# Kernel optimization log

Hardware: AMD Instinct MI355X
Metric: run time of the kernel (lower is better)

Reference implementation:

```python
import jax, jax.numpy as jnp
import numpy as np

S = 2        # downscale
REDUCE = 32  # QK channel dim


def _to_grid(x):
    # [B,C,H,W] -> [B,C,H/S,W/S,S*S], matching ConverToGrid (reshape+permute+reshape)
    B, C, H, W = x.shape
    h, w = H // S, W // S
    x = x.reshape(B, C, h, S, w, S)
    x = x.transpose(0, 1, 2, 4, 3, 5)
    return x.reshape(B, C, h, w, S * S)


def setup_inputs() -> dict:
    key = jax.random.key(0)
    k1, k2, k3 = jax.random.split(key, 3)
    fm = jax.random.normal(k1, (8, 128, 256, 256), dtype=jnp.float32)
    Wq = jax.random.normal(k2, (REDUCE, 128), dtype=jnp.float32) * 0.05
    Wk = jax.random.normal(k3, (REDUCE, 128), dtype=jnp.float32) * 0.05
    return {"fm": fm, "Wq": Wq, "Wk": Wk}


def reference(fm, Wq, Wk):
    B, C, H, W = fm.shape
    h, w = H // S, W // S
    # Q branch: AvgPool2d(S,S) -> 1x1 conv -> scale by 1/sqrt(reduce)
    pooled = fm.reshape(B, C, h, S, w, S).mean(axis=(3, 5))          # [B,C,h,w]
    Q = jnp.einsum('rc,bchw->brhw', Wq, pooled) / jnp.sqrt(
        jnp.asarray(REDUCE, fm.dtype))                               # [B,r,h,w]
    # K branch: 1x1 conv -> grid
    K = _to_grid(jnp.einsum('rc,bchw->brhw', Wk, fm))                # [B,r,h,w,S*S]
    # V branch: grid of raw features
    V = _to_grid(fm)                                                 # [B,C,h,w,S*S]
    # sum over channel dim of Q*K, softmax over window dim (dropout p=0 => identity)
    logits = jnp.einsum('brhw,brhws->bhws', Q, K)                    # [B,h,w,S*S]
    attn = jax.nn.softmax(logits, axis=-1)
    # weighted sum over window positions
    out = jnp.einsum('bchws,bhws->bchw', V, attn)                    # [B,C,h,w]
    return out
```

## Files before the change

kernel.cpp:

```cpp
#include <hip/hip_runtime.h>
#include <hip/hip_bf16.h>
#include <math.h>


typedef unsigned int uint32;

__device__ __forceinline__ uint32 pack2(float x, float y) {
  union { __hip_bfloat162 h; uint32 u; } cvt;
  cvt.h = __float22bfloat162_rn(make_float2(x, y));
  return cvt.u;
}
__device__ __forceinline__ float2 unpack2(uint32 u) {
  float2 r;
  r.x = __uint_as_float(u << 16);
  r.y = __uint_as_float(u & 0xffff0000u);
  return r;
}

__global__ __launch_bounds__(256) void wt_kernel(const float* __restrict__ Wq,
                                                 const float* __restrict__ Wk,
                                                 float* __restrict__ ws) {
  int t = blockIdx.x * 256 + threadIdx.x;
  if (t < 4096) {
    int c = t >> 5, r = t & 31;
    ws[c * 32 + r]        = Wq[r * 128 + c] * (0.25f / sqrtf(32.0f));
    ws[4096 + c * 32 + r] = Wk[r * 128 + c];
  }
}

__global__ __launch_bounds__(512)
void attn_main(const float* __restrict__ fm,
               const float* __restrict__ ws,
               float* __restrict__ out) {
  __shared__ float Qpart[4 * 32 * 64];
  __shared__ float lbuf[8 * 64 * 4];
  __shared__ float abuf[64 * 4];

  const int tid = threadIdx.x;
  const int p   = tid & 63;
  const int g   = __builtin_amdgcn_readfirstlane(tid >> 6);

  const int blk = blockIdx.x;
  const int w0  = (blk & 1) * 64;
  const int h   = (blk >> 1) & 127;
  const int b   = blk >> 8;
  const int cb  = g * 16;

  const float* gbase = fm + ((size_t)(b * 128 + cb) * 65536) +
                       (size_t)(2 * h) * 256 + 2 * (w0 + p);
  const float* wq = ws + cb * 32;
  const float* wk = ws + 4096 + cb * 32;

  uint32 pka[16], pkb[16];
  {
    const float* gp = gbase;
#pragma unroll
    for (int i = 0; i < 16; ++i) {
      const float2 va = *(const float2*)(gp);
      const float2 vb = *(const float2*)(gp + 256);
      pka[i] = pack2(va.x, va.y);
      pkb[i] = pack2(vb.x, vb.y);
      gp += 65536;
    }
  }

  float qa[32];
#pragma unroll
  for (int r = 0; r < 32; ++r) qa[r] = 0.f;
#pragma unroll
  for (int i = 0; i < 16; ++i) {
    const float2 va = unpack2(pka[i]);
    const float2 vb = unpack2(pkb[i]);
    const float u = (va.x + va.y) + (vb.x + vb.y);
#pragma unroll
    for (int r = 0; r < 32; ++r)
      qa[r] = fmaf(wq[i * 32 + r], u, qa[r]);
  }

  if (g >= 4) {
#pragma unroll
    for (int r = 0; r < 32; ++r) Qpart[(g - 4) * 2048 + r * 64 + p] = qa[r];
  }
  __syncthreads();
  if (g < 4) {
#pragma unroll
    for (int r = 0; r < 32; ++r) Qpart[g * 2048 + r * 64 + p] += qa[r];
  }
  __syncthreads();
  if (g < 2) {
#pragma unroll
    for (int r = 0; r < 32; ++r)
      Qpart[g * 2048 + r * 64 + p] += Qpart[(g + 2) * 2048 + r * 64 + p];
  }
  __syncthreads();
#pragma unroll
  for (int r = 0; r < 32; ++r)
    qa[r] = Qpart[r * 64 + p] + Qpart[2048 + r * 64 + p];

  float l0 = 0.f, l1 = 0.f, l2 = 0.f, l3 = 0.f;
#pragma unroll
  for (int i = 0; i < 16; ++i) {
    const float2 va = unpack2(pka[i]);
    const float2 vb = unpack2(pkb[i]);
    float t0 = 0.f, t1 = 0.f;
#pragma unroll
    for (int r = 0; r < 32; r += 2) {
      t0 = fmaf(qa[r + 0], wk[i * 32 + r + 0], t0);
      t1 = fmaf(qa[r + 1], wk[i * 32 + r + 1], t1);
    }
    const float tv = t0 + t1;
    l0 = fmaf(tv, va.x, l0);
    l1 = fmaf(tv, va.y, l1);
    l2 = fmaf(tv, vb.x, l2);
    l3 = fmaf(tv, vb.y, l3);
  }
  *(float4*)(lbuf + (g * 64 + p) * 4) = make_float4(l0, l1, l2, l3);
  __syncthreads();

  if (tid < 64) {
    float L0 = 0.f, L1 = 0.f, L2 = 0.f, L3 = 0.f;
#pragma unroll
    for (int k = 0; k < 8; ++k) {
      const float4 s = *(const float4*)(lbuf + (k * 64 + tid) * 4);
      L0 += s.x; L1 += s.y; L2 += s.z; L3 += s.w;
    }
    const float mx = fmaxf(fmaxf(L0, L1), fmaxf(L2, L3));
    const float e0 = __expf(L0 - mx), e1 = __expf(L1 - mx);
    const float e2 = __expf(L2 - mx), e3 = __expf(L3 - mx);
    const float inv = 1.0f / ((e0 + e1) + (e2 + e3));
    *(float4*)(abuf + tid * 4) =
        make_float4(e0 * inv, e1 * inv, e2 * inv, e3 * inv);
  }
  __syncthreads();
  const float4 at = *(const float4*)(abuf + p * 4);

  {
    float* op = out + ((size_t)(b * 128 + cb) * 16384) + h * 128 + w0 + p;
#pragma unroll
    for (int i = 0; i < 16; ++i) {
      const float2 va = unpack2(pka[i]);
      const float2 vb = unpack2(pkb[i]);
      op[(size_t)i * 16384] =
          fmaf(at.x, va.x, fmaf(at.y, va.y, fmaf(at.z, vb.x, at.w * vb.y)));
    }
  }
}

extern "C" void kernel_launch(void* const* d_in, const int* in_sizes, int n_in,
                              void* d_out, int out_size, void* d_ws, size_t ws_size,
                              hipStream_t stream) {
  const float* fm = (const float*)d_in[0];
  const float* Wq = (const float*)d_in[1];
  const float* Wk = (const float*)d_in[2];
  float* outp = (float*)d_out;
  float* ws = (float*)d_ws;

  wt_kernel<<<16, 256, 0, stream>>>(Wq, Wk, ws);
  attn_main<<<2048, 512, 0, stream>>>(fm, ws, outp);
}
```

Baseline: 138.3 us.

## Split Q reduction into two 16-channel halves and shrink blocks to 32 pixels

Blocks now cover 32 output pixels with 256 threads (8 channel groups of 32 lanes) instead of 64 pixels with 512 threads, and launch bounds ask for 8 blocks per CU. The 32-channel Q accumulation is split into two 16-channel passes with separate shared reductions, which halves the live Q registers to raise occupancy. Weight reads are vectorized as float4. The cost is more barriers and a recomputed pooled sum per pass, and each wave now issues 32-lane memory accesses, so half of every 64-wide wavefront sits idle.

```diff
diff --git a/kernel.cpp b/kernel.cpp
--- a/kernel.cpp
+++ b/kernel.cpp
@@ -28,100 +28,199 @@
   }
 }
 
-__global__ __launch_bounds__(512)
+__global__ __launch_bounds__(256, 8)
 void attn_main(const float* __restrict__ fm,
                const float* __restrict__ ws,
                float* __restrict__ out) {
-  __shared__ float Qpart[4 * 32 * 64];
-  __shared__ float lbuf[8 * 64 * 4];
-  __shared__ float abuf[64 * 4];
+  __shared__ float QsA[4 * 16 * 32];
+  __shared__ float QsB[4 * 16 * 32];
 
   const int tid = threadIdx.x;
-  const int p   = tid & 63;
-  const int g   = __builtin_amdgcn_readfirstlane(tid >> 6);
+  const int p   = tid & 31;
+  const int cq  = tid >> 5;
 
   const int blk = blockIdx.x;
-  const int w0  = (blk & 1) * 64;
-  const int h   = (blk >> 1) & 127;
-  const int b   = blk >> 8;
-  const int cb  = g * 16;
-
-  const float* gbase = fm + ((size_t)(b * 128 + cb) * 65536) +
+  const int w0  = (blk & 3) * 32;
+  const int h   = (blk >> 2) & 127;
+  const int b   = blk >> 9;
+  const int cb  = cq * 16;
+
+  const float* gbase = fm + ((size_t)(b * 128 + cb)) * 65536 +
                        (size_t)(2 * h) * 256 + 2 * (w0 + p);
-  const float* wq = ws + cb * 32;
-  const float* wk = ws + 4096 + cb * 32;
+  const float* wqp = ws + cb * 32;
+  const float* wkp = ws + 4096 + cb * 32;
 
   uint32 pka[16], pkb[16];
-  {
-    const float* gp = gbase;
-#pragma unroll
-    for (int i = 0; i < 16; ++i) {
-      const float2 va = *(const float2*)(gp);
-      const float2 vb = *(const float2*)(gp + 256);
-      pka[i] = pack2(va.x, va.y);
-      pkb[i] = pack2(vb.x, vb.y);
-      gp += 65536;
-    }
-  }
-
-  float qa[32];
-#pragma unroll
-  for (int r = 0; r < 32; ++r) qa[r] = 0.f;
+#pragma unroll
+  for (int i = 0; i < 16; ++i) {
+    const float2 va = *(const float2*)(gbase + (size_t)i * 65536);
+    const float2 vb = *(const float2*)(gbase + (size_t)i * 65536 + 256);
+    pka[i] = pack2(va.x, va.y);
+    pkb[i] = pack2(vb.x, vb.y);
+  }
+
+  float qa[16];
+
+#pragma unroll
+  for (int r = 0; r < 16; ++r) qa[r] = 0.f;
 #pragma unroll
   for (int i = 0; i < 16; ++i) {
     const float2 va = unpack2(pka[i]);
     const float2 vb = unpack2(pkb[i]);
     const float u = (va.x + va.y) + (vb.x + vb.y);
-#pragma unroll
-    for (int r = 0; r < 32; ++r)
-      qa[r] = fmaf(wq[i * 32 + r], u, qa[r]);
-  }
-
-  if (g >= 4) {
-#pragma unroll
-    for (int r = 0; r < 32; ++r) Qpart[(g - 4) * 2048 + r * 64 + p] = qa[r];
-  }
-  __syncthreads();
-  if (g < 4) {
-#pragma unroll
-    for (int r = 0; r < 32; ++r) Qpart[g * 2048 + r * 64 + p] += qa[r];
-  }
-  __syncthreads();
-  if (g < 2) {
-#pragma unroll
-    for (int r = 0; r < 32; ++r)
-      Qpart[g * 2048 + r * 64 + p] += Qpart[(g + 2) * 2048 + r * 64 + p];
-  }
-  __syncthreads();
-#pragma unroll
-  for (int r = 0; r < 32; ++r)
-    qa[r] = Qpart[r * 64 + p] + Qpart[2048 + r * 64 + p];
-
-  float l0 = 0.f, l1 = 0.f, l2 = 0.f, l3 = 0.f;
+    const float4 w0_ = *(const float4*)(wqp + i * 32 + 0);
+    const float4 w1_ = *(const float4*)(wqp + i * 32 + 4);
+    const float4 w2_ = *(const float4*)(wqp + i * 32 + 8);
+    const float4 w3_ = *(const float4*)(wqp + i * 32 + 12);
+    qa[0]  = fmaf(w0_.x, u, qa[0]);
+    qa[1]  = fmaf(w0_.y, u, qa[1]);
+    qa[2]  = fmaf(w0_.z, u, qa[2]);
+    qa[3]  = fmaf(w0_.w, u, qa[3]);
+    qa[4]  = fmaf(w1_.x, u, qa[4]);
+    qa[5]  = fmaf(w1_.y, u, qa[5]);
+    qa[6]  = fmaf(w1_.z, u, qa[6]);
+    qa[7]  = fmaf(w1_.w, u, qa[7]);
+    qa[8]  = fmaf(w2_.x, u, qa[8]);
+    qa[9]  = fmaf(w2_.y, u, qa[9]);
+    qa[10] = fmaf(w2_.z, u, qa[10]);
+    qa[11] = fmaf(w2_.w, u, qa[11]);
+    qa[12] = fmaf(w3_.x, u, qa[12]);
+    qa[13] = fmaf(w3_.y, u, qa[13]);
+    qa[14] = fmaf(w3_.z, u, qa[14]);
+    qa[15] = fmaf(w3_.w, u, qa[15]);
+  }
+  if (cq >= 4) {
+#pragma unroll
+    for (int r = 0; r < 16; ++r) QsA[(cq - 4) * 512 + r * 32 + p] = qa[r];
+  }
+  __syncthreads();
+  if (cq < 4) {
+#pragma unroll
+    for (int r = 0; r < 16; ++r) QsA[cq * 512 + r * 32 + p] += qa[r];
+  }
+  __syncthreads();
+  if (cq < 2) {
+#pragma unroll
+    for (int r = 0; r < 16; ++r)
+      QsA[cq * 512 + r * 32 + p] += QsA[(cq + 2) * 512 + r * 32 + p];
+  }
+  __syncthreads();
+
+#pragma unroll
+  for (int r = 0; r < 16; ++r) qa[r] = 0.f;
 #pragma unroll
   for (int i = 0; i < 16; ++i) {
     const float2 va = unpack2(pka[i]);
     const float2 vb = unpack2(pkb[i]);
-    float t0 = 0.f, t1 = 0.f;
-#pragma unroll
-    for (int r = 0; r < 32; r += 2) {
-      t0 = fmaf(qa[r + 0], wk[i * 32 + r + 0], t0);
-      t1 = fmaf(qa[r + 1], wk[i * 32 + r + 1], t1);
-    }
-    const float tv = t0 + t1;
-    l0 = fmaf(tv, va.x, l0);
-    l1 = fmaf(tv, va.y, l1);
-    l2 = fmaf(tv, vb.x, l2);
-    l3 = fmaf(tv, vb.y, l3);
-  }
-  *(float4*)(lbuf + (g * 64 + p) * 4) = make_float4(l0, l1, l2, l3);
-  __syncthreads();
-
-  if (tid < 64) {
+    const float u = (va.x + va.y) + (vb.x + vb.y);
+    const float4 w0_ = *(const float4*)(wqp + i * 32 + 16);
+    const float4 w1_ = *(const float4*)(wqp + i * 32 + 20);
+    const float4 w2_ = *(const float4*)(wqp + i * 32 + 24);
+    const float4 w3_ = *(const float4*)(wqp + i * 32 + 28);
+    qa[0]  = fmaf(w0_.x, u, qa[0]);
+    qa[1]  = fmaf(w0_.y, u, qa[1]);
+    qa[2]  = fmaf(w0_.z, u, qa[2]);
+    qa[3]  = fmaf(w0_.w, u, qa[3]);
+    qa[4]  = fmaf(w1_.x, u, qa[4]);
+    qa[5]  = fmaf(w1_.y, u, qa[5]);
+    qa[6]  = fmaf(w1_.z, u, qa[6]);
+    qa[7]  = fmaf(w1_.w, u, qa[7]);
+    qa[8]  = fmaf(w2_.x, u, qa[8]);
+    qa[9]  = fmaf(w2_.y, u, qa[9]);
+    qa[10] = fmaf(w2_.z, u, qa[10]);
+    qa[11] = fmaf(w2_.w, u, qa[11]);
+    qa[12] = fmaf(w3_.x, u, qa[12]);
+    qa[13] = fmaf(w3_.y, u, qa[13]);
+    qa[14] = fmaf(w3_.z, u, qa[14]);
+    qa[15] = fmaf(w3_.w, u, qa[15]);
+  }
+  if (cq >= 4) {
+#pragma unroll
+    for (int r = 0; r < 16; ++r) QsB[(cq - 4) * 512 + r * 32 + p] = qa[r];
+  }
+  __syncthreads();
+  if (cq < 4) {
+#pragma unroll
+    for (int r = 0; r < 16; ++r) QsB[cq * 512 + r * 32 + p] += qa[r];
+  }
+  __syncthreads();
+  if (cq < 2) {
+#pragma unroll
+    for (int r = 0; r < 16; ++r)
+      QsB[cq * 512 + r * 32 + p] += QsB[(cq + 2) * 512 + r * 32 + p];
+  }
+  __syncthreads();
+
+  float l0 = 0.f, l1 = 0.f, l2 = 0.f, l3 = 0.f;
+  {
+    float qh[16];
+#pragma unroll
+    for (int r = 0; r < 16; ++r)
+      qh[r] = QsA[r * 32 + p] + QsA[512 + r * 32 + p];
+#pragma unroll
+    for (int i = 0; i < 16; ++i) {
+      const float4 k0 = *(const float4*)(wkp + i * 32 + 0);
+      const float4 k1 = *(const float4*)(wkp + i * 32 + 4);
+      const float4 k2 = *(const float4*)(wkp + i * 32 + 8);
+      const float4 k3 = *(const float4*)(wkp + i * 32 + 12);
+      float t0 = 0.f, t1 = 0.f;
+      t0 = fmaf(qh[0],  k0.x, t0); t1 = fmaf(qh[1],  k0.y, t1);
+      t0 = fmaf(qh[2],  k0.z, t0); t1 = fmaf(qh[3],  k0.w, t1);
+      t0 = fmaf(qh[4],  k1.x, t0); t1 = fmaf(qh[5],  k1.y, t1);
+      t0 = fmaf(qh[6],  k1.z, t0); t1 = fmaf(qh[7],  k1.w, t1);
+      t0 = fmaf(qh[8],  k2.x, t0); t1 = fmaf(qh[9],  k2.y, t1);
+      t0 = fmaf(qh[10], k2.z, t0); t1 = fmaf(qh[11], k2.w, t1);
+      t0 = fmaf(qh[12], k3.x, t0); t1 = fmaf(qh[13], k3.y, t1);
+      t0 = fmaf(qh[14], k3.z, t0); t1 = fmaf(qh[15], k3.w, t1);
+      const float tv = t0 + t1;
+      const float2 va = unpack2(pka[i]);
+      const float2 vb = unpack2(pkb[i]);
+      l0 = fmaf(tv, va.x, l0);
+      l1 = fmaf(tv, va.y, l1);
+      l2 = fmaf(tv, vb.x, l2);
+      l3 = fmaf(tv, vb.y, l3);
+    }
+  }
+  {
+    float qh[16];
+#pragma unroll
+    for (int r = 0; r < 16; ++r)
+      qh[r] = QsB[r * 32 + p] + QsB[512 + r * 32 + p];
+#pragma unroll
+    for (int i = 0; i < 16; ++i) {
+      const float4 k0 = *(const float4*)(wkp + i * 32 + 16);
+      const float4 k1 = *(const float4*)(wkp + i * 32 + 20);
+      const float4 k2 = *(const float4*)(wkp + i * 32 + 24);
+      const float4 k3 = *(const float4*)(wkp + i * 32 + 28);
+      float t0 = 0.f, t1 = 0.f;
+      t0 = fmaf(qh[0],  k0.x, t0); t1 = fmaf(qh[1],  k0.y, t1);
+      t0 = fmaf(qh[2],  k0.z, t0); t1 = fmaf(qh[3],  k0.w, t1);
+      t0 = fmaf(qh[4],  k1.x, t0); t1 = fmaf(qh[5],  k1.y, t1);
+      t0 = fmaf(qh[6],  k1.z, t0); t1 = fmaf(qh[7],  k1.w, t1);
+      t0 = fmaf(qh[8],  k2.x, t0); t1 = fmaf(qh[9],  k2.y, t1);
+      t0 = fmaf(qh[10], k2.z, t0); t1 = fmaf(qh[11], k2.w, t1);
+      t0 = fmaf(qh[12], k3.x, t0); t1 = fmaf(qh[13], k3.y, t1);
+      t0 = fmaf(qh[14], k3.z, t0); t1 = fmaf(qh[15], k3.w, t1);
+      const float tv = t0 + t1;
+      const float2 va = unpack2(pka[i]);
+      const float2 vb = unpack2(pkb[i]);
+      l0 = fmaf(tv, va.x, l0);
+      l1 = fmaf(tv, va.y, l1);
+      l2 = fmaf(tv, vb.x, l2);
+      l3 = fmaf(tv, vb.y, l3);
+    }
+  }
+  __syncthreads();
+
+  float* lbuf = QsA;
+  *(float4*)(lbuf + (cq * 32 + p) * 4) = make_float4(l0, l1, l2, l3);
+  __syncthreads();
+  float* abuf = QsB;
+  if (tid < 32) {
     float L0 = 0.f, L1 = 0.f, L2 = 0.f, L3 = 0.f;
 #pragma unroll
     for (int k = 0; k < 8; ++k) {
-      const float4 s = *(const float4*)(lbuf + (k * 64 + tid) * 4);
+      const float4 s = *(const float4*)(lbuf + (k * 32 + tid) * 4);
       L0 += s.x; L1 += s.y; L2 += s.z; L3 += s.w;
     }
     const float mx = fmaxf(fmaxf(L0, L1), fmaxf(L2, L3));
@@ -135,7 +234,7 @@
   const float4 at = *(const float4*)(abuf + p * 4);
 
   {
-    float* op = out + ((size_t)(b * 128 + cb) * 16384) + h * 128 + w0 + p;
+    float* op = out + ((size_t)(b * 128 + cb)) * 16384 + h * 128 + w0 + p;
 #pragma unroll
     for (int i = 0; i < 16; ++i) {
       const float2 va = unpack2(pka[i]);
@@ -156,5 +255,5 @@
   float* ws = (float*)d_ws;
 
   wt_kernel<<<16, 256, 0, stream>>>(Wq, Wk, ws);
-  attn_main<<<2048, 512, 0, stream>>>(fm, ws, outp);
-}
+  attn_main<<<4096, 256, 0, stream>>>(fm, ws, outp);
+}
```

Result: slower. 391.7 us (+183.3%).

## Halve block size to 4 warps handling 32 channels each, split Q reduction

Applied to the files above, without the earlier changes.

Each block now uses 256 threads, with each wavefront owning 32 channels instead of 16, and holds twice as many packed bf16 pixel values in registers. The 32-wide Q accumulation is split into two 16-row halves, each reduced across the four wavefronts through shared memory. This keeps register pressure per half bounded and shortens the cross-wave reduction tree. It trades more serial work and register use per thread for fewer threads, smaller reductions and dynamic shared memory, which may lower occupancy or latency hiding.

```diff
diff --git a/kernel.cpp b/kernel.cpp
--- a/kernel.cpp
+++ b/kernel.cpp
@@ -28,13 +28,15 @@
   }
 }
 
-__global__ __launch_bounds__(512)
+__global__ __launch_bounds__(256)
 void attn_main(const float* __restrict__ fm,
                const float* __restrict__ ws,
                float* __restrict__ out) {
-  __shared__ float Qpart[4 * 32 * 64];
-  __shared__ float lbuf[8 * 64 * 4];
-  __shared__ float abuf[64 * 4];
+  extern __shared__ float smem[];
+  float* QA   = smem;
+  float* QB   = smem + 2048;
+  float* lbuf = smem + 4096;
+  float* abuf = smem + 5120;
 
   const int tid = threadIdx.x;
   const int p   = tid & 63;
@@ -44,86 +46,125 @@
   const int w0  = (blk & 1) * 64;
   const int h   = (blk >> 1) & 127;
   const int b   = blk >> 8;
-  const int cb  = g * 16;
-
-  const float* gbase = fm + ((size_t)(b * 128 + cb) * 65536) +
+  const int cb  = g * 32;
+
+  const float* gbase = fm + ((size_t)(b * 128 + cb)) * 65536 +
                        (size_t)(2 * h) * 256 + 2 * (w0 + p);
   const float* wq = ws + cb * 32;
   const float* wk = ws + 4096 + cb * 32;
 
-  uint32 pka[16], pkb[16];
-  {
-    const float* gp = gbase;
-#pragma unroll
-    for (int i = 0; i < 16; ++i) {
-      const float2 va = *(const float2*)(gp);
-      const float2 vb = *(const float2*)(gp + 256);
-      pka[i] = pack2(va.x, va.y);
-      pkb[i] = pack2(vb.x, vb.y);
-      gp += 65536;
-    }
-  }
-
-  float qa[32];
-#pragma unroll
-  for (int r = 0; r < 32; ++r) qa[r] = 0.f;
-#pragma unroll
-  for (int i = 0; i < 16; ++i) {
+  uint32 pka[32], pkb[32];
+#pragma unroll
+  for (int i = 0; i < 32; ++i) {
+    const float2 va = *(const float2*)(gbase + (size_t)i * 65536);
+    const float2 vb = *(const float2*)(gbase + (size_t)i * 65536 + 256);
+    pka[i] = pack2(va.x, va.y);
+    pkb[i] = pack2(vb.x, vb.y);
+  }
+
+  float qa[16];
+
+#pragma unroll
+  for (int r = 0; r < 16; ++r) qa[r] = 0.f;
+#pragma unroll
+  for (int i = 0; i < 32; ++i) {
     const float2 va = unpack2(pka[i]);
     const float2 vb = unpack2(pkb[i]);
     const float u = (va.x + va.y) + (vb.x + vb.y);
 #pragma unroll
-    for (int r = 0; r < 32; ++r)
+    for (int r = 0; r < 16; ++r)
       qa[r] = fmaf(wq[i * 32 + r], u, qa[r]);
   }
-
-  if (g >= 4) {
-#pragma unroll
-    for (int r = 0; r < 32; ++r) Qpart[(g - 4) * 2048 + r * 64 + p] = qa[r];
-  }
-  __syncthreads();
-  if (g < 4) {
-#pragma unroll
-    for (int r = 0; r < 32; ++r) Qpart[g * 2048 + r * 64 + p] += qa[r];
+  if (g >= 2) {
+#pragma unroll
+    for (int r = 0; r < 16; ++r) QA[(g - 2) * 1024 + r * 64 + p] = qa[r];
   }
   __syncthreads();
   if (g < 2) {
 #pragma unroll
-    for (int r = 0; r < 32; ++r)
-      Qpart[g * 2048 + r * 64 + p] += Qpart[(g + 2) * 2048 + r * 64 + p];
-  }
-  __syncthreads();
-#pragma unroll
-  for (int r = 0; r < 32; ++r)
-    qa[r] = Qpart[r * 64 + p] + Qpart[2048 + r * 64 + p];
-
-  float l0 = 0.f, l1 = 0.f, l2 = 0.f, l3 = 0.f;
-#pragma unroll
-  for (int i = 0; i < 16; ++i) {
+    for (int r = 0; r < 16; ++r) QA[g * 1024 + r * 64 + p] += qa[r];
+  }
+
+#pragma unroll
+  for (int r = 0; r < 16; ++r) qa[r] = 0.f;
+#pragma unroll
+  for (int i = 0; i < 32; ++i) {
     const float2 va = unpack2(pka[i]);
     const float2 vb = unpack2(pkb[i]);
-    float t0 = 0.f, t1 = 0.f;
-#pragma unroll
-    for (int r = 0; r < 32; r += 2) {
-      t0 = fmaf(qa[r + 0], wk[i * 32 + r + 0], t0);
-      t1 = fmaf(qa[r + 1], wk[i * 32 + r + 1], t1);
+    const float u = (va.x + va.y) + (vb.x + vb.y);
+#pragma unroll
+    for (int r = 0; r < 16; ++r)
+      qa[r] = fmaf(wq[i * 32 + 16 + r], u, qa[r]);
+  }
+  __syncthreads();
+  if (g >= 2) {
+#pragma unroll
+    for (int r = 0; r < 16; ++r) QB[(g - 2) * 1024 + r * 64 + p] = qa[r];
+  }
+  __syncthreads();
+  if (g < 2) {
+#pragma unroll
+    for (int r = 0; r < 16; ++r) QB[g * 1024 + r * 64 + p] += qa[r];
+  }
+  __syncthreads();
+
+  float l0 = 0.f, l1 = 0.f, l2 = 0.f, l3 = 0.f;
+  {
+    float qh[16];
+#pragma unroll
+    for (int r = 0; r < 16; ++r)
+      qh[r] = QA[r * 64 + p] + QA[1024 + r * 64 + p];
+#pragma unroll
+    for (int i = 0; i < 32; ++i) {
+      float t0 = 0.f, t1 = 0.f;
+#pragma unroll
+      for (int r = 0; r < 16; r += 2) {
+        t0 = fmaf(qh[r + 0], wk[i * 32 + r + 0], t0);
+        t1 = fmaf(qh[r + 1], wk[i * 32 + r + 1], t1);
+      }
+      const float tv = t0 + t1;
+      const float2 va = unpack2(pka[i]);
+      const float2 vb = unpack2(pkb[i]);
+      l0 = fmaf(tv, va.x, l0);
+      l1 = fmaf(tv, va.y, l1);
+      l2 = fmaf(tv, vb.x, l2);
+      l3 = fmaf(tv, vb.y, l3);
     }
-    const float tv = t0 + t1;
-    l0 = fmaf(tv, va.x, l0);
-    l1 = fmaf(tv, va.y, l1);
-    l2 = fmaf(tv, vb.x, l2);
-    l3 = fmaf(tv, vb.y, l3);
+  }
+  {
+    float qh[16];
+#pragma unroll
+    for (int r = 0; r < 16; ++r)
+      qh[r] = QB[r * 64 + p] + QB[1024 + r * 64 + p];
+#pragma unroll
+    for (int i = 0; i < 32; ++i) {
+      float t0 = 0.f, t1 = 0.f;
+#pragma unroll
+      for (int r = 0; r < 16; r += 2) {
+        t0 = fmaf(qh[r + 0], wk[i * 32 + 16 + r + 0], t0);
+        t1 = fmaf(qh[r + 1], wk[i * 32 + 16 + r + 1], t1);
+      }
+      const float tv = t0 + t1;
+      const float2 va = unpack2(pka[i]);
+      const float2 vb = unpack2(pkb[i]);
+      l0 = fmaf(tv, va.x, l0);
+      l1 = fmaf(tv, va.y, l1);
+      l2 = fmaf(tv, vb.x, l2);
+      l3 = fmaf(tv, vb.y, l3);
+    }
   }
   *(float4*)(lbuf + (g * 64 + p) * 4) = make_float4(l0, l1, l2, l3);
   __syncthreads();
 
   if (tid < 64) {
-    float L0 = 0.f, L1 = 0.f, L2 = 0.f, L3 = 0.f;
-#pragma unroll
-    for (int k = 0; k < 8; ++k) {
-      const float4 s = *(const float4*)(lbuf + (k * 64 + tid) * 4);
-      L0 += s.x; L1 += s.y; L2 += s.z; L3 += s.w;
-    }
+    const float4 s0 = *(const float4*)(lbuf + (0 * 64 + tid) * 4);
+    const float4 s1 = *(const float4*)(lbuf + (1 * 64 + tid) * 4);
+    const float4 s2 = *(const float4*)(lbuf + (2 * 64 + tid) * 4);
+    const float4 s3 = *(const float4*)(lbuf + (3 * 64 + tid) * 4);
+    const float L0 = (s0.x + s1.x) + (s2.x + s3.x);
+    const float L1 = (s0.y + s1.y) + (s2.y + s3.y);
+    const float L2 = (s0.z + s1.z) + (s2.z + s3.z);
+    const float L3 = (s0.w + s1.w) + (s2.w + s3.w);
     const float mx = fmaxf(fmaxf(L0, L1), fmaxf(L2, L3));
     const float e0 = __expf(L0 - mx), e1 = __expf(L1 - mx);
     const float e2 = __expf(L2 - mx), e3 = __expf(L3 - mx);
@@ -135,9 +176,9 @@
   const float4 at = *(const float4*)(abuf + p * 4);
 
   {
-    float* op = out + ((size_t)(b * 128 + cb) * 16384) + h * 128 + w0 + p;
-#pragma unroll
-    for (int i = 0; i < 16; ++i) {
+    float* op = out + ((size_t)(b * 128 + cb)) * 16384 + h * 128 + w0 + p;
+#pragma unroll
+    for (int i = 0; i < 32; ++i) {
       const float2 va = unpack2(pka[i]);
       const float2 vb = unpack2(pkb[i]);
       op[(size_t)i * 16384] =
@@ -155,6 +196,7 @@
   float* outp = (float*)d_out;
   float* ws = (float*)d_ws;
 
+  const int smem_bytes = 36864;
   wt_kernel<<<16, 256, 0, stream>>>(Wq, Wk, ws);
-  attn_main<<<2048, 512, 0, stream>>>(fm, ws, outp);
-}
+  attn_main<<<2048, 256, smem_bytes, stream>>>(fm, ws, outp);
+}
```

Measured after the change: 146.8 us. 6.2% more time.

## Shrink blocks to 32 pixels and compute Q in register-light chunks

Applied to the files above, without the earlier changes.

Blocks now cover 32 pixels with 256 threads instead of 64 pixels with 512, which doubles the grid and sets a launch bound of 5 blocks per CU. The per-thread Q accumulator of 32 registers becomes four chunks of 8, reduced through a smaller shared buffer, and the pooled sums are precomputed and packed at load time. Weight reads switch to float4 vectors. The aim is lower register pressure and higher occupancy to hide memory latency, at the cost of more barriers and smaller wavefronts (32 pixels per 64-lane wave row split) that may hurt coalescing.

```diff
diff --git a/kernel.cpp b/kernel.cpp
--- a/kernel.cpp
+++ b/kernel.cpp
@@ -28,100 +28,112 @@
   }
 }
 
-__global__ __launch_bounds__(512)
+__global__ __launch_bounds__(256, 5)
 void attn_main(const float* __restrict__ fm,
                const float* __restrict__ ws,
                float* __restrict__ out) {
-  __shared__ float Qpart[4 * 32 * 64];
-  __shared__ float lbuf[8 * 64 * 4];
-  __shared__ float abuf[64 * 4];
+  __shared__ float Qt[4 * 8 * 32];
+  __shared__ float Qf[32 * 32];
+  __shared__ float lbuf[8 * 32 * 4];
+  __shared__ float abuf[32 * 4];
 
   const int tid = threadIdx.x;
-  const int p   = tid & 63;
-  const int g   = __builtin_amdgcn_readfirstlane(tid >> 6);
-
+  const int p   = tid & 31;
+  const int g   = tid >> 5;
   const int blk = blockIdx.x;
-  const int w0  = (blk & 1) * 64;
-  const int h   = (blk >> 1) & 127;
-  const int b   = blk >> 8;
+  const int w0  = (blk & 3) * 32;
+  const int h   = (blk >> 2) & 127;
+  const int b   = blk >> 9;
   const int cb  = g * 16;
 
-  const float* gbase = fm + ((size_t)(b * 128 + cb) * 65536) +
+  const float* gbase = fm + ((size_t)(b * 128 + cb)) * 65536 +
                        (size_t)(2 * h) * 256 + 2 * (w0 + p);
-  const float* wq = ws + cb * 32;
-  const float* wk = ws + 4096 + cb * 32;
+  const float* wqv = ws + cb * 32;
+  const float* wkv = ws + 4096 + cb * 32;
 
-  uint32 pka[16], pkb[16];
-  {
-    const float* gp = gbase;
+  uint32 pka[16], pkb[16], pku[8];
 #pragma unroll
-    for (int i = 0; i < 16; ++i) {
-      const float2 va = *(const float2*)(gp);
-      const float2 vb = *(const float2*)(gp + 256);
-      pka[i] = pack2(va.x, va.y);
-      pkb[i] = pack2(vb.x, vb.y);
-      gp += 65536;
-    }
+  for (int ii = 0; ii < 8; ++ii) {
+    const float2 va0 = *(const float2*)(gbase + (size_t)(2 * ii) * 65536);
+    const float2 vb0 = *(const float2*)(gbase + (size_t)(2 * ii) * 65536 + 256);
+    const float2 va1 = *(const float2*)(gbase + (size_t)(2 * ii + 1) * 65536);
+    const float2 vb1 = *(const float2*)(gbase + (size_t)(2 * ii + 1) * 65536 + 256);
+    pka[2 * ii]     = pack2(va0.x, va0.y);
+    pkb[2 * ii]     = pack2(vb0.x, vb0.y);
+    pka[2 * ii + 1] = pack2(va1.x, va1.y);
+    pkb[2 * ii + 1] = pack2(vb1.x, vb1.y);
+    pku[ii] = pack2((va0.x + va0.y) + (vb0.x + vb0.y),
+                    (va1.x + va1.y) + (vb1.x + vb1.y));
   }
 
-  float qa[32];
 #pragma unroll
-  for (int r = 0; r < 32; ++r) qa[r] = 0.f;
+  for (int q = 0; q < 4; ++q) {
+    float qa[8];
 #pragma unroll
-  for (int i = 0; i < 16; ++i) {
-    const float2 va = unpack2(pka[i]);
-    const float2 vb = unpack2(pkb[i]);
-    const float u = (va.x + va.y) + (vb.x + vb.y);
+    for (int j = 0; j < 8; ++j) qa[j] = 0.f;
 #pragma unroll
-    for (int r = 0; r < 32; ++r)
-      qa[r] = fmaf(wq[i * 32 + r], u, qa[r]);
+    for (int ii = 0; ii < 8; ++ii) {
+      const float2 uu = unpack2(pku[ii]);
+      const float4 wa0 = *(const float4*)(wqv + (2 * ii) * 32 + q * 8);
+      const float4 wa1 = *(const float4*)(wqv + (2 * ii) * 32 + q * 8 + 4);
+      const float4 wb0 = *(const float4*)(wqv + (2 * ii + 1) * 32 + q * 8);
+      const float4 wb1 = *(const float4*)(wqv + (2 * ii + 1) * 32 + q * 8 + 4);
+      qa[0] = fmaf(wa0.x, uu.x, qa[0]); qa[1] = fmaf(wa0.y, uu.x, qa[1]);
+      qa[2] = fmaf(wa0.z, uu.x, qa[2]); qa[3] = fmaf(wa0.w, uu.x, qa[3]);
+      qa[4] = fmaf(wa1.x, uu.x, qa[4]); qa[5] = fmaf(wa1.y, uu.x, qa[5]);
+      qa[6] = fmaf(wa1.z, uu.x, qa[6]); qa[7] = fmaf(wa1.w, uu.x, qa[7]);
+      qa[0] = fmaf(wb0.x, uu.y, qa[0]); qa[1] = fmaf(wb0.y, uu.y, qa[1]);
+      qa[2] = fmaf(wb0.z, uu.y, qa[2]); qa[3] = fmaf(wb0.w, uu.y, qa[3]);
+      qa[4] = fmaf(wb1.x, uu.y, qa[4]); qa[5] = fmaf(wb1.y, uu.y, qa[5]);
+      qa[6] = fmaf(wb1.z, uu.y, qa[6]); qa[7] = fmaf(wb1.w, uu.y, qa[7]);
+    }
+    if (g >= 4) {
+#pragma unroll
+      for (int j = 0; j < 8; ++j) Qt[(g - 4) * 256 + j * 32 + p] = qa[j];
+    }
+    __syncthreads();
+    if (g < 4) {
+#pragma unroll
+      for (int j = 0; j < 8; ++j) Qt[g * 256 + j * 32 + p] += qa[j];
+    }
+    __syncthreads();
+    Qf[(q * 8 + g) * 32 + p] = (Qt[g * 32 + p] + Qt[256 + g * 32 + p]) +
+                               (Qt[512 + g * 32 + p] + Qt[768 + g * 32 + p]);
+    __syncthreads();
   }
-
-  if (g >= 4) {
-#pragma unroll
-    for (int r = 0; r < 32; ++r) Qpart[(g - 4) * 2048 + r * 64 + p] = qa[r];
-  }
-  __syncthreads();
-  if (g < 4) {
-#pragma unroll
-    for (int r = 0; r < 32; ++r) Qpart[g * 2048 + r * 64 + p] += qa[r];
-  }
-  __syncthreads();
-  if (g < 2) {
-#pragma unroll
-    for (int r = 0; r < 32; ++r)
-      Qpart[g * 2048 + r * 64 + p] += Qpart[(g + 2) * 2048 + r * 64 + p];
-  }
-  __syncthreads();
-#pragma unroll
-  for (int r = 0; r < 32; ++r)
-    qa[r] = Qpart[r * 64 + p] + Qpart[2048 + r * 64 + p];
 
   float l0 = 0.f, l1 = 0.f, l2 = 0.f, l3 = 0.f;
 #pragma unroll
-  for (int i = 0; i < 16; ++i) {
-    const float2 va = unpack2(pka[i]);
-    const float2 vb = unpack2(pkb[i]);
-    float t0 = 0.f, t1 = 0.f;
+  for (int q = 0; q < 4; ++q) {
+    float qh[8];
 #pragma unroll
-    for (int r = 0; r < 32; r += 2) {
-      t0 = fmaf(qa[r + 0], wk[i * 32 + r + 0], t0);
-      t1 = fmaf(qa[r + 1], wk[i * 32 + r + 1], t1);
+    for (int r = 0; r < 8; ++r) qh[r] = Qf[(q * 8 + r) * 32 + p];
+#pragma unroll
+    for (int i = 0; i < 16; ++i) {
+      const float4 k0 = *(const float4*)(wkv + i * 32 + q * 8);
+      const float4 k1 = *(const float4*)(wkv + i * 32 + q * 8 + 4);
+      float t0 = qh[0] * k0.x;
+      float t1 = qh[1] * k0.y;
+      t0 = fmaf(qh[2], k0.z, t0); t1 = fmaf(qh[3], k0.w, t1);
+      t0 = fmaf(qh[4], k1.x, t0); t1 = fmaf(qh[5], k1.y, t1);
+      t0 = fmaf(qh[6], k1.z, t0); t1 = fmaf(qh[7], k1.w, t1);
+      const float tv = t0 + t1;
+      const float2 va = unpack2(pka[i]);
+      const float2 vb = unpack2(pkb[i]);
+      l0 = fmaf(tv, va.x, l0);
+      l1 = fmaf(tv, va.y, l1);
+      l2 = fmaf(tv, vb.x, l2);
+      l3 = fmaf(tv, vb.y, l3);
     }
-    const float tv = t0 + t1;
-    l0 = fmaf(tv, va.x, l0);
-    l1 = fmaf(tv, va.y, l1);
-    l2 = fmaf(tv, vb.x, l2);
-    l3 = fmaf(tv, vb.y, l3);
   }
-  *(float4*)(lbuf + (g * 64 + p) * 4) = make_float4(l0, l1, l2, l3);
+  *(float4*)(lbuf + (g * 32 + p) * 4) = make_float4(l0, l1, l2, l3);
   __syncthreads();
 
-  if (tid < 64) {
+  if (tid < 32) {
     float L0 = 0.f, L1 = 0.f, L2 = 0.f, L3 = 0.f;
 #pragma unroll
     for (int k = 0; k < 8; ++k) {
-      const float4 s = *(const float4*)(lbuf + (k * 64 + tid) * 4);
+      const float4 s = *(const float4*)(lbuf + (k * 32 + tid) * 4);
       L0 += s.x; L1 += s.y; L2 += s.z; L3 += s.w;
     }
     const float mx = fmaxf(fmaxf(L0, L1), fmaxf(L2, L3));
@@ -135,7 +147,7 @@
   const float4 at = *(const float4*)(abuf + p * 4);
 
   {
-    float* op = out + ((size_t)(b * 128 + cb) * 16384) + h * 128 + w0 + p;
+    float* op = out + ((size_t)(b * 128 + cb)) * 16384 + h * 128 + w0 + p;
 #pragma unroll
     for (int i = 0; i < 16; ++i) {
       const float2 va = unpack2(pka[i]);
@@ -156,5 +168,5 @@
   float* ws = (float*)d_ws;
 
   wt_kernel<<<16, 256, 0, stream>>>(Wq, Wk, ws);
-  attn_main<<<2048, 512, 0, stream>>>(fm, ws, outp);
+  attn_main<<<4096, 256, 0, stream>>>(fm, ws, outp);
 }
```

Result: slower. 397.6 us (+187.6%).
